# Kernel optimization log

Hardware: AMD Instinct MI355X
Metric: run time of the kernel (lower is better)

## Reference

```python
import jax, jax.numpy as jnp
import numpy as np

NX, NY, NZ = 64, 48, 32          # grid_resolution
N = NX * NY * NZ                 # 98304 grid cells
P = 10                           # neighbors_in_radius
D = 3                            # spatial dims
M = 5                            # num_modes (fourier)
BN = 64                          # base_neurons
BN_IN = 8                        # base_neurons_in (output channels)
IN_FEAT = D * (1 + 2 * M)        # 33


def _linear_init(k, fan_in, fan_out):
    s = 1.0 / np.sqrt(fan_in)
    kw, kb = jax.random.split(k)
    W = jax.random.uniform(kw, (fan_in, fan_out), jnp.float32, -s, s)
    b = jax.random.uniform(kb, (fan_out,), jnp.float32, -s, s)
    return W, b


def setup_inputs() -> dict:
    key = jax.random.key(0)
    ks = jax.random.split(key, 6)
    # neighbor point coordinates gathered by ball query: (b, N, P, 3)
    x = jax.random.normal(ks[0], (1, N, P, D), jnp.float32)
    # regular grid coordinates: (b, nx, ny, nz, 3)
    grid = jax.random.normal(ks[1], (1, NX, NY, NZ, D), jnp.float32)
    # fourier frequency buffer: exp(linspace(0, pi, num_modes))
    freqs = jnp.exp(jnp.linspace(0.0, float(np.pi), M)).astype(jnp.float32)
    W1, b1 = _linear_init(ks[2], IN_FEAT, BN)
    W2, b2 = _linear_init(ks[3], BN, BN // 2)
    W3, b3 = _linear_init(ks[4], BN // 2, BN_IN)
    return dict(x=x, grid=grid, freqs=freqs,
                W1=W1, b1=b1, W2=W2, b2=b2, W3=W3, b3=b3)


def _fourier_encode(coords, freqs):
    # coords: (b, N, P, D), freqs: (F,)
    scaled = coords[..., None, :] * freqs[:, None]          # (b, N, P, F, D)
    b, n, p = coords.shape[:3]
    scaled = scaled.reshape(b, n, p, -1)                    # (b, N, P, F*D)
    return jnp.concatenate([jnp.sin(scaled), jnp.cos(scaled)], axis=-1)


def reference(x, grid, freqs, W1, b1, W2, b2, W3, b3):
    gelu = lambda t: jax.nn.gelu(t, approximate=False)  # torch F.gelu default = exact erf
    # Fourier feature encode neighbor coords: (b, N, P, 33)
    facets = jnp.concatenate([x, _fourier_encode(x, freqs)], axis=-1)
    h = gelu(facets @ W1 + b1)                              # (b, N, P, 64)
    h = gelu(h @ W2 + b2)                                   # (b, N, P, 32)
    h = jnp.tanh(h @ W3 + b3)                               # (b, N, P, 8)
    # mask out padded neighbors (zero coords); original uses x-coordinate channel
    mask = (jnp.abs(x[..., 0:1]) > 1e-6).astype(h.dtype)    # (b, N, P, 1)
    out = jnp.sum(h * mask, axis=2)                         # scatter/aggregate -> (b, N, 8)
    out = out.reshape(out.shape[0], NX, NY, NZ, BN_IN)
    return jnp.transpose(out, (0, 4, 1, 2, 3))              # (b, 8, nx, ny, nz)
```

## Files before the change

### kernel.cpp

```cpp
#include <hip/hip_runtime.h>
#include <math.h>

#define NXD 64
#define NYD 48
#define NZD 32
#define NPT (NXD*NYD*NZD)
#define PN  10
#define MF  5
#define H1  64
#define H2  32
#define H3  8

#define PTS_PER_BLOCK 32
#define ROWS_PER_BLOCK (PTS_PER_BLOCK*PN)
#define TILES_PER_WAVE 5

#define A2S 72
#define A3S 40

#define INV2PI 0.15915494309189535f

typedef __attribute__((ext_vector_type(8))) _Float16 half8;
typedef __attribute__((ext_vector_type(2))) _Float16 half2v;
typedef __attribute__((ext_vector_type(2))) __fp16   fp16x2;
typedef __attribute__((ext_vector_type(2))) short    shortv2;
typedef __attribute__((ext_vector_type(4))) float    f32x4;

__device__ __forceinline__ half2v cvt_pk_h2(float lo, float hi) {
    fp16x2 p = __builtin_amdgcn_cvt_pkrtz(lo, hi);
    return __builtin_bit_cast(half2v, p);
}

static __device__ const unsigned short kSlotTab[32] = {
  2048,    3,   70,  137,  204,  271, 1042, 1109,
  2561, 1176, 1243, 1310,  516,  583,  650,  717,
  2562,  272, 1043, 1110, 1177, 1244, 1311,  517,
    72,  139,  206,  273, 1044, 1111, 1178, 1245 };

__device__ __forceinline__ _Float16 exp2h(_Float16 v) {
    _Float16 r;
    asm("v_exp_f16 %0, %1" : "=v"(r) : "v"(v));
    return r;
}

__device__ __forceinline__ half2v gelu_pk(float lo, float hi) {
    const _Float16 C1 = (_Float16)2.3022082f, C2 = (_Float16)0.10294324f;
    const half2v x  = cvt_pk_h2(lo, hi);
    const half2v x2 = x * x;
    half2v t = x * __builtin_elementwise_fma(x2, (half2v){C2, C2}, (half2v){C1, C1});
    t = __builtin_elementwise_min(t, (half2v){(_Float16)14.0f, (_Float16)14.0f});
    const _Float16 e0 = exp2h(t[0]);
    const _Float16 e1 = exp2h(t[1]);
    const half2v one = {(_Float16)1.0f, (_Float16)1.0f};
    const half2v two = {(_Float16)2.0f, (_Float16)2.0f};
    const half2v y = (half2v){e0, e1} + one;
    const shortv2 rb = (shortv2){(short)0x7800, (short)0x7800} - __builtin_bit_cast(shortv2, y);
    half2v r = __builtin_bit_cast(half2v, rb);
    r = r * __builtin_elementwise_fma(-y, r, two);
    r = r * __builtin_elementwise_fma(-y, r, two);
    return x - x * r;
}

__device__ __forceinline__ float tanh_fast(float v) {
    float E = __builtin_amdgcn_exp2f(2.8853901f * v);
    return 1.0f - 2.0f * __builtin_amdgcn_rcpf(E + 1.0f);
}

__global__ __launch_bounds__(256) void domino_mfma_kernel(
    const float* __restrict__ x,
    const float* __restrict__ freqs,
    const float* __restrict__ W1,
    const float* __restrict__ b1,
    const float* __restrict__ W2,
    const float* __restrict__ b2,
    const float* __restrict__ W3,
    const float* __restrict__ b3,
    float* __restrict__ out)
{
    __shared__ __align__(16) _Float16 a2buf[4][2][16 * A2S];
    __shared__ __align__(16) float cbuf[976];
    __shared__ __align__(16) _Float16 obuf[ROWS_PER_BLOCK * 9];
    __shared__ __align__(16) float mcx[4][2][16];
    __shared__ __align__(16) float mv32[4][2][16];
    __shared__ __align__(16) float coefA[2][32];
    __shared__ __align__(16) float coefB[2][32];
    __shared__ __align__(16) float coefO[2][32];

    const int tid  = threadIdx.x;
    const int w    = tid >> 6;
    const int lane = tid & 63;
    const int lr   = lane & 15;
    const int lg   = lane >> 4;

    const int wrow0 = blockIdx.x * ROWS_PER_BLOCK + w * (TILES_PER_WAVE*16);

    if (tid < 32) {
        const unsigned e = kSlotTab[tid];
        const int m = (e >> 6) & 7, path = (e >> 9) & 1, ty = (e >> 10) & 3;
        const float fm = freqs[m] * INV2PI;
        const float fa = (ty != 2 && path == 0) ? fm : 0.0f;
        const float fb = (ty != 2 && path == 1) ? fm : 0.0f;
        const float fo = (ty == 1) ? 0.25f : 0.0f;
        coefA[0][tid] = fa; coefA[1][tid] = fa;
        coefB[0][tid] = fb; coefB[1][tid] = fb;
        coefO[0][tid] = fo; coefO[1][tid] = fo;
    }

    {
        const int sl = (w == 3 && lane >= 60) ? 59 : lane;
        const float* gsrc = x + (size_t)wrow0 * 3 + (size_t)sl * 4;
        __builtin_amdgcn_global_load_lds(
            (const __attribute__((address_space(1))) void*)gsrc,
            (__attribute__((address_space(3))) void*)&cbuf[w * 240], 16, 0, 0);
    }

    const float f4rev = freqs[4] * INV2PI;
    const float rawf  = (lg < 3) ? 1.0f : 0.0f;

    half8 B1f[4];
    float  w32[4], bv1[4];
    #pragma unroll
    for (int t1 = 0; t1 < 4; ++t1) {
        #pragma unroll
        for (int j = 0; j < 8; ++j) {
            const int row = kSlotTab[lg*8 + j] & 63;
            B1f[t1][j] = (_Float16)W1[row*H1 + t1*16 + lr];
        }
        w32[t1] = W1[32*H1 + t1*16 + lr];
        bv1[t1] = b1[t1*16 + lr];
    }
    half8 B2f[2][2];
    float  bv2[2];
    #pragma unroll
    for (int s = 0; s < 2; ++s)
        #pragma unroll
        for (int t2 = 0; t2 < 2; ++t2)
            #pragma unroll
            for (int j = 0; j < 8; ++j)
                B2f[s][t2][j] = (_Float16)W2[(s*32 + lg*8 + j)*H2 + t2*16 + lr];
    #pragma unroll
    for (int t2 = 0; t2 < 2; ++t2) bv2[t2] = b2[t2*16 + lr];

    half8 B3f;
    float  bv3 = (lr < H3) ? b3[lr] : 0.0f;
    #pragma unroll
    for (int j = 0; j < 8; ++j)
        B3f[j] = (lr < H3) ? (_Float16)W3[(lg*8 + j)*H3 + lr] : (_Float16)0.0f;

    __syncthreads();

    auto featgen = [&](int t, int u,
                       const f32x4& fa0, const f32x4& fb0, const f32x4& fo0,
                       const f32x4& fa1, const f32x4& fb1, const f32x4& fo1) -> half8 {
        const int cfx = w*240 + (t*16 + lr)*3;
        const float cx = cbuf[cfx + 0];
        const float cy = cbuf[cfx + 1];
        const float cz = cbuf[cfx + 2];
        const float cA = (lg <= 1) ? cx : ((lg == 2) ? cy : cz);
        const float cB = (lg == 0) ? cx : ((lg == 1) ? cy : cz);
        float fv[8];
        #pragma unroll
        for (int j = 0; j < 4; ++j) {
            float rev = cA*fa0[j] + (cB*fb0[j] + fo0[j]);
            fv[j] = __builtin_amdgcn_sinf(__builtin_amdgcn_fractf(rev));
        }
        #pragma unroll
        for (int j = 0; j < 4; ++j) {
            float rev = cA*fa1[j] + (cB*fb1[j] + fo1[j]);
            fv[4+j] = __builtin_amdgcn_sinf(__builtin_amdgcn_fractf(rev));
        }
        fv[0] += rawf * (cB - fv[0]);
        if (lg == 0) {
            mcx[w][u][lr]  = cx;
            mv32[w][u][lr] = __builtin_amdgcn_sinf(__builtin_amdgcn_fractf(cz * f4rev + 0.25f));
        }
        union { half2v h2[4]; half8 h8; } a1u;
        #pragma unroll
        for (int j = 0; j < 4; ++j)
            a1u.h2[j] = cvt_pk_h2(fv[2*j], fv[2*j+1]);
        return a1u.h8;
    };

    auto layer1 = [&](const half8& a1, f32x4* c1, int u) {
        #pragma unroll
        for (int t1 = 0; t1 < 4; ++t1) {
            f32x4 ci = {bv1[t1], bv1[t1], bv1[t1], bv1[t1]};
            c1[t1] = __builtin_amdgcn_mfma_f32_16x16x32_f16(a1, B1f[t1], ci, 0, 0, 0);
        }
        const f32x4 v32r = *(const f32x4*)&mv32[w][u][lg*4];
        #pragma unroll
        for (int t1 = 0; t1 < 4; ++t1)
            #pragma unroll
            for (int r = 0; r < 4; ++r)
                c1[t1][r] += v32r[r] * w32[t1];
    };

    auto gelu_a2 = [&](const f32x4* c1, int u) {
        _Float16* const buf = &a2buf[w][u][0];
        #pragma unroll
        for (int t1 = 0; t1 < 4; ++t1) {
            const half2v g01 = gelu_pk(c1[t1][0], c1[t1][1]);
            const half2v g23 = gelu_pk(c1[t1][2], c1[t1][3]);
            const int col = t1*16 + lr;
            buf[(lg*4 + 0)*A2S + col] = g01[0];
            buf[(lg*4 + 1)*A2S + col] = g01[1];
            buf[(lg*4 + 2)*A2S + col] = g23[0];
            buf[(lg*4 + 3)*A2S + col] = g23[1];
        }
    };

    auto read_a2 = [&](int u, half8* a2f) {
        #pragma unroll
        for (int s = 0; s < 2; ++s)
            a2f[s] = *(const half8*)&a2buf[w][u][lr*A2S + s*32 + lg*8];
    };

    auto layer2 = [&](const half8* a2f, f32x4* c2) {
        #pragma unroll
        for (int t2 = 0; t2 < 2; ++t2) {
            f32x4 ci = {bv2[t2], bv2[t2], bv2[t2], bv2[t2]};
            ci = __builtin_amdgcn_mfma_f32_16x16x32_f16(a2f[0], B2f[0][t2], ci, 0, 0, 0);
            c2[t2] = __builtin_amdgcn_mfma_f32_16x16x32_f16(a2f[1], B2f[1][t2], ci, 0, 0, 0);
        }
    };

    auto gelu_a3 = [&](const f32x4* c2, int u) {
        _Float16* const a3p = &a2buf[w][u][0];
        #pragma unroll
        for (int t2 = 0; t2 < 2; ++t2) {
            const half2v g01 = gelu_pk(c2[t2][0], c2[t2][1]);
            const half2v g23 = gelu_pk(c2[t2][2], c2[t2][3]);
            const int col = t2*16 + lr;
            a3p[(lg*4 + 0)*A3S + col] = g01[0];
            a3p[(lg*4 + 1)*A3S + col] = g01[1];
            a3p[(lg*4 + 2)*A3S + col] = g23[0];
            a3p[(lg*4 + 3)*A3S + col] = g23[1];
        }
    };

    auto l3_tail = [&](int t, int u) {
        const half8 a3f = *(const half8*)&a2buf[w][u][lr*A3S + lg*8];
        f32x4 c3 = {bv3, bv3, bv3, bv3};
        c3 = __builtin_amdgcn_mfma_f32_16x16x32_f16(a3f, B3f, c3, 0, 0, 0);
        const f32x4 mxr = *(const f32x4*)&mcx[w][u][lg*4];
        #pragma unroll
        for (int r = 0; r < 4; ++r) {
            const int brow = w*(TILES_PER_WAVE*16) + t*16 + lg*4 + r;
            const float mk = (fabsf(mxr[r]) > 1e-6f) ? 1.0f : 0.0f;
            if (lr < H3) obuf[brow*9 + lr] = (_Float16)(mk * tanh_fast(c3[r]));
        }
    };

    #pragma unroll 1
    for (int tp = 0; tp < 2; ++tp) {
        const int tc = tp & 1;
        const f32x4 fa0 = *(const f32x4*)&coefA[tc][lg*8];
        const f32x4 fb0 = *(const f32x4*)&coefB[tc][lg*8];
        const f32x4 fo0 = *(const f32x4*)&coefO[tc][lg*8];
        const f32x4 fa1 = *(const f32x4*)&coefA[tc][lg*8 + 4];
        const f32x4 fb1 = *(const f32x4*)&coefB[tc][lg*8 + 4];
        const f32x4 fo1 = *(const f32x4*)&coefO[tc][lg*8 + 4];

        const half8 a1a = featgen(2*tp + 0, 0, fa0, fb0, fo0, fa1, fb1, fo1);
        const half8 a1b = featgen(2*tp + 1, 1, fa0, fb0, fo0, fa1, fb1, fo1);

        f32x4 c1a[4], c1b[4];
        layer1(a1a, c1a, 0);
        layer1(a1b, c1b, 1);

        gelu_a2(c1a, 0);
        gelu_a2(c1b, 1);

        half8 a2fa[2], a2fb[2];
        read_a2(0, a2fa);
        read_a2(1, a2fb);

        f32x4 c2a[2], c2b[2];
        layer2(a2fa, c2a);
        layer2(a2fb, c2b);

        gelu_a3(c2a, 0);
        gelu_a3(c2b, 1);

        l3_tail(2*tp + 0, 0);
        l3_tail(2*tp + 1, 1);
    }

    {
        const f32x4 fa0 = *(const f32x4*)&coefA[0][lg*8];
        const f32x4 fb0 = *(const f32x4*)&coefB[0][lg*8];
        const f32x4 fo0 = *(const f32x4*)&coefO[0][lg*8];
        const f32x4 fa1 = *(const f32x4*)&coefA[0][lg*8 + 4];
        const f32x4 fb1 = *(const f32x4*)&coefB[0][lg*8 + 4];
        const f32x4 fo1 = *(const f32x4*)&coefO[0][lg*8 + 4];

        const half8 a1t = featgen(4, 0, fa0, fb0, fo0, fa1, fb1, fo1);
        f32x4 c1t[4];
        layer1(a1t, c1t, 0);
        gelu_a2(c1t, 0);
        half8 a2ft[2];
        read_a2(0, a2ft);
        f32x4 c2t[2];
        layer2(a2ft, c2t);
        gelu_a3(c2t, 0);
        l3_tail(4, 0);
    }

    __syncthreads();

    {
        const int p  = tid >> 3;
        const int ch = tid & 7;
        float sum = 0.0f;
        #pragma unroll
        for (int i = 0; i < PN; ++i) sum += (float)obuf[(p*PN + i)*9 + ch];
        const int gp = blockIdx.x * PTS_PER_BLOCK + p;
        out[(size_t)ch * NPT + gp] = sum;
    }
}

extern "C" void kernel_launch(void* const* d_in, const int* in_sizes, int n_in,
                              void* d_out, int out_size, void* d_ws, size_t ws_size,
                              hipStream_t stream) {
    const float* x     = (const float*)d_in[0];
    const float* freqs = (const float*)d_in[2];
    const float* W1    = (const float*)d_in[3];
    const float* b1    = (const float*)d_in[4];
    const float* W2    = (const float*)d_in[5];
    const float* b2    = (const float*)d_in[6];
    const float* W3    = (const float*)d_in[7];
    const float* b3    = (const float*)d_in[8];
    float* out = (float*)d_out;

    const int grid = NPT / PTS_PER_BLOCK;
    domino_mfma_kernel<<<grid, 256, 0, stream>>>(x, freqs, W1, b1, W2, b2, W3, b3, out);
}
```

Before: 122.7 us.

## Process three point chunks per block with double-buffered coordinate prefetch

Each block now handles three 32-point chunks in sequence instead of one, and the grid shrinks to a third of its former size. The coordinates for the next chunk are fetched into a second LDS buffer while the current chunk is computed. The per-block setup is paid once per three chunks: converting the weight fragments to fp16 into registers and building the Fourier coefficient tables. Launch bounds now request 4 blocks per SM. The risks are a single wave of blocks with less latency hiding and tail balancing, and an extra barrier per chunk.

```diff
diff --git a/kernel.cpp b/kernel.cpp
--- a/kernel.cpp
+++ b/kernel.cpp
@@ -12,6 +12,7 @@
 #define H3  8
 
 #define PTS_PER_BLOCK 32
+#define CHUNKS 3
 #define ROWS_PER_BLOCK (PTS_PER_BLOCK*PN)
 #define TILES_PER_WAVE 5
 
@@ -66,7 +67,7 @@
     return 1.0f - 2.0f * __builtin_amdgcn_rcpf(E + 1.0f);
 }
 
-__global__ __launch_bounds__(256) void domino_mfma_kernel(
+__global__ __launch_bounds__(256, 4) void domino_mfma_kernel(
     const float* __restrict__ x,
     const float* __restrict__ freqs,
     const float* __restrict__ W1,
@@ -78,7 +79,7 @@
     float* __restrict__ out)
 {
     __shared__ __align__(16) _Float16 a2buf[4][2][16 * A2S];
-    __shared__ __align__(16) float cbuf[976];
+    __shared__ __align__(16) float cbuf[2][976];
     __shared__ __align__(16) _Float16 obuf[ROWS_PER_BLOCK * 9];
     __shared__ __align__(16) float mcx[4][2][16];
     __shared__ __align__(16) float mv32[4][2][16];
@@ -92,7 +93,14 @@
     const int lr   = lane & 15;
     const int lg   = lane >> 4;
 
-    const int wrow0 = blockIdx.x * ROWS_PER_BLOCK + w * (TILES_PER_WAVE*16);
+    auto stage_coords = [&](int c, int buf) {
+        const int row0 = (blockIdx.x*CHUNKS + c) * ROWS_PER_BLOCK + w*(TILES_PER_WAVE*16);
+        const int sl = (w == 3 && lane >= 60) ? 59 : lane;
+        const float* gsrc = x + (size_t)row0 * 3 + (size_t)sl * 4;
+        __builtin_amdgcn_global_load_lds(
+            (const __attribute__((address_space(1))) void*)gsrc,
+            (__attribute__((address_space(3))) void*)&cbuf[buf][w * 240], 16, 0, 0);
+    };
 
     if (tid < 32) {
         const unsigned e = kSlotTab[tid];
@@ -106,13 +114,7 @@
         coefO[0][tid] = fo; coefO[1][tid] = fo;
     }
 
-    {
-        const int sl = (w == 3 && lane >= 60) ? 59 : lane;
-        const float* gsrc = x + (size_t)wrow0 * 3 + (size_t)sl * 4;
-        __builtin_amdgcn_global_load_lds(
-            (const __attribute__((address_space(1))) void*)gsrc,
-            (__attribute__((address_space(3))) void*)&cbuf[w * 240], 16, 0, 0);
-    }
+    stage_coords(0, 0);
 
     const float f4rev = freqs[4] * INV2PI;
     const float rawf  = (lg < 3) ? 1.0f : 0.0f;
@@ -149,13 +151,13 @@
 
     __syncthreads();
 
-    auto featgen = [&](int t, int u,
+    auto featgen = [&](const float* cbp, int t, int u,
                        const f32x4& fa0, const f32x4& fb0, const f32x4& fo0,
                        const f32x4& fa1, const f32x4& fb1, const f32x4& fo1) -> half8 {
         const int cfx = w*240 + (t*16 + lr)*3;
-        const float cx = cbuf[cfx + 0];
-        const float cy = cbuf[cfx + 1];
-        const float cz = cbuf[cfx + 2];
+        const float cx = cbp[cfx + 0];
+        const float cy = cbp[cfx + 1];
+        const float cz = cbp[cfx + 2];
         const float cA = (lg <= 1) ? cx : ((lg == 2) ? cy : cz);
         const float cB = (lg == 0) ? cx : ((lg == 1) ? cy : cz);
         float fv[8];
@@ -252,70 +254,78 @@
     };
 
     #pragma unroll 1
-    for (int tp = 0; tp < 2; ++tp) {
-        const int tc = tp & 1;
-        const f32x4 fa0 = *(const f32x4*)&coefA[tc][lg*8];
-        const f32x4 fb0 = *(const f32x4*)&coefB[tc][lg*8];
-        const f32x4 fo0 = *(const f32x4*)&coefO[tc][lg*8];
-        const f32x4 fa1 = *(const f32x4*)&coefA[tc][lg*8 + 4];
-        const f32x4 fb1 = *(const f32x4*)&coefB[tc][lg*8 + 4];
-        const f32x4 fo1 = *(const f32x4*)&coefO[tc][lg*8 + 4];
-
-        const half8 a1a = featgen(2*tp + 0, 0, fa0, fb0, fo0, fa1, fb1, fo1);
-        const half8 a1b = featgen(2*tp + 1, 1, fa0, fb0, fo0, fa1, fb1, fo1);
-
-        f32x4 c1a[4], c1b[4];
-        layer1(a1a, c1a, 0);
-        layer1(a1b, c1b, 1);
-
-        gelu_a2(c1a, 0);
-        gelu_a2(c1b, 1);
-
-        half8 a2fa[2], a2fb[2];
-        read_a2(0, a2fa);
-        read_a2(1, a2fb);
-
-        f32x4 c2a[2], c2b[2];
-        layer2(a2fa, c2a);
-        layer2(a2fb, c2b);
-
-        gelu_a3(c2a, 0);
-        gelu_a3(c2b, 1);
-
-        l3_tail(2*tp + 0, 0);
-        l3_tail(2*tp + 1, 1);
-    }
-
-    {
-        const f32x4 fa0 = *(const f32x4*)&coefA[0][lg*8];
-        const f32x4 fb0 = *(const f32x4*)&coefB[0][lg*8];
-        const f32x4 fo0 = *(const f32x4*)&coefO[0][lg*8];
-        const f32x4 fa1 = *(const f32x4*)&coefA[0][lg*8 + 4];
-        const f32x4 fb1 = *(const f32x4*)&coefB[0][lg*8 + 4];
-        const f32x4 fo1 = *(const f32x4*)&coefO[0][lg*8 + 4];
-
-        const half8 a1t = featgen(4, 0, fa0, fb0, fo0, fa1, fb1, fo1);
-        f32x4 c1t[4];
-        layer1(a1t, c1t, 0);
-        gelu_a2(c1t, 0);
-        half8 a2ft[2];
-        read_a2(0, a2ft);
-        f32x4 c2t[2];
-        layer2(a2ft, c2t);
-        gelu_a3(c2t, 0);
-        l3_tail(4, 0);
-    }
-
-    __syncthreads();
-
-    {
-        const int p  = tid >> 3;
-        const int ch = tid & 7;
-        float sum = 0.0f;
-        #pragma unroll
-        for (int i = 0; i < PN; ++i) sum += (float)obuf[(p*PN + i)*9 + ch];
-        const int gp = blockIdx.x * PTS_PER_BLOCK + p;
-        out[(size_t)ch * NPT + gp] = sum;
+    for (int c = 0; c < CHUNKS; ++c) {
+        if (c + 1 < CHUNKS) stage_coords(c + 1, (c + 1) & 1);
+        const float* cbp = &cbuf[c & 1][0];
+
+        #pragma unroll 1
+        for (int tp = 0; tp < 2; ++tp) {
+            const int tc = tp & 1;
+            const f32x4 fa0 = *(const f32x4*)&coefA[tc][lg*8];
+            const f32x4 fb0 = *(const f32x4*)&coefB[tc][lg*8];
+            const f32x4 fo0 = *(const f32x4*)&coefO[tc][lg*8];
+            const f32x4 fa1 = *(const f32x4*)&coefA[tc][lg*8 + 4];
+            const f32x4 fb1 = *(const f32x4*)&coefB[tc][lg*8 + 4];
+            const f32x4 fo1 = *(const f32x4*)&coefO[tc][lg*8 + 4];
+
+            const half8 a1a = featgen(cbp, 2*tp + 0, 0, fa0, fb0, fo0, fa1, fb1, fo1);
+            const half8 a1b = featgen(cbp, 2*tp + 1, 1, fa0, fb0, fo0, fa1, fb1, fo1);
+
+            f32x4 c1a[4], c1b[4];
+            layer1(a1a, c1a, 0);
+            layer1(a1b, c1b, 1);
+
+            gelu_a2(c1a, 0);
+            gelu_a2(c1b, 1);
+
+            half8 a2fa[2], a2fb[2];
+            read_a2(0, a2fa);
+            read_a2(1, a2fb);
+
+            f32x4 c2a[2], c2b[2];
+            layer2(a2fa, c2a);
+            layer2(a2fb, c2b);
+
+            gelu_a3(c2a, 0);
+            gelu_a3(c2b, 1);
+
+            l3_tail(2*tp + 0, 0);
+            l3_tail(2*tp + 1, 1);
+        }
+
+        {
+            const f32x4 fa0 = *(const f32x4*)&coefA[0][lg*8];
+            const f32x4 fb0 = *(const f32x4*)&coefB[0][lg*8];
+            const f32x4 fo0 = *(const f32x4*)&coefO[0][lg*8];
+            const f32x4 fa1 = *(const f32x4*)&coefA[0][lg*8 + 4];
+            const f32x4 fb1 = *(const f32x4*)&coefB[0][lg*8 + 4];
+            const f32x4 fo1 = *(const f32x4*)&coefO[0][lg*8 + 4];
+
+            const half8 a1t = featgen(cbp, 4, 0, fa0, fb0, fo0, fa1, fb1, fo1);
+            f32x4 c1t[4];
+            layer1(a1t, c1t, 0);
+            gelu_a2(c1t, 0);
+            half8 a2ft[2];
+            read_a2(0, a2ft);
+            f32x4 c2t[2];
+            layer2(a2ft, c2t);
+            gelu_a3(c2t, 0);
+            l3_tail(4, 0);
+        }
+
+        __syncthreads();
+
+        {
+            const int p  = tid >> 3;
+            const int ch = tid & 7;
+            float sum = 0.0f;
+            #pragma unroll
+            for (int i = 0; i < PN; ++i) sum += (float)obuf[(p*PN + i)*9 + ch];
+            const int gp = blockIdx.x * (PTS_PER_BLOCK*CHUNKS) + c*PTS_PER_BLOCK + p;
+            out[(size_t)ch * NPT + gp] = sum;
+        }
+
+        if (c + 1 < CHUNKS) __syncthreads();
     }
 }
 
@@ -332,6 +342,6 @@
     const float* b3    = (const float*)d_in[8];
     float* out = (float*)d_out;
 
-    const int grid = NPT / PTS_PER_BLOCK;
+    const int grid = NPT / (PTS_PER_BLOCK * CHUNKS);
     domino_mfma_kernel<<<grid, 256, 0, stream>>>(x, freqs, W1, b1, W2, b2, W3, b3, out);
 }
```

Measured after the change: 124.2 us. No clear change (+1.2%).
